# Performance work log

Measured on AMD Instinct MI355X. Metric: run time of the kernel, lower is better.

## Reference

```python
import jax, jax.numpy as jnp
import numpy as np

IDIM, HDIM, ODIM, G = 80, 512, 128, 5
B, T = 512, 512  # B = scan (time) axis of torch GRU (batch_first=False), T = GRU batch axis
P = G * 2 * ODIM + G  # 1285


def setup_inputs() -> dict:
    key = jax.random.key(0)
    ks = jax.random.split(key, 8)
    s = 0.05  # keep recurrent dynamics stable
    return {
        "ys": jax.random.normal(ks[0], (B, T, IDIM), jnp.float32),
        "W_ih": jax.random.normal(ks[1], (3 * HDIM, IDIM), jnp.float32) * s,
        "W_hh": jax.random.normal(ks[2], (3 * HDIM, HDIM), jnp.float32) * s,
        "b_ih": jax.random.normal(ks[3], (3 * HDIM,), jnp.float32) * s,
        "b_hh": jax.random.normal(ks[4], (3 * HDIM,), jnp.float32) * s,
        "W_proj": jax.random.normal(ks[5], (P, HDIM), jnp.float32) * s,
        "b_proj": jax.random.normal(ks[6], (P,), jnp.float32) * s,
        "eps": jax.random.normal(ks[7], (G, B, ODIM), jnp.float32),  # pre-drawn std-normal noise per component
    }


def _gru(ys, W_ih, W_hh, b_ih, b_hh):
    # torch GRU, batch_first=False: scan over axis 0 of ys, batch = axis 1.
    xp = jnp.einsum('btf,gf->btg', ys, W_ih) + b_ih  # (B, T, 3H), precomputed input projections
    h0 = jnp.zeros((ys.shape[1], HDIM), ys.dtype)

    def step(h, x):
        gh = h @ W_hh.T + b_hh
        xr, xz, xn = jnp.split(x, 3, axis=-1)
        hr, hz, hn = jnp.split(gh, 3, axis=-1)
        r = jax.nn.sigmoid(xr + hr)
        z = jax.nn.sigmoid(xz + hz)
        n = jnp.tanh(xn + r * hn)
        h_new = (1.0 - z) * n + z * h
        return h_new, h_new

    _, out = jax.lax.scan(step, h0, xp)  # (B, T, H)
    return out


def reference(ys, W_ih, W_hh, b_ih, b_hh, W_proj, b_proj, eps):
    out = _gru(ys, W_ih, W_hh, b_ih, b_hh)          # (B, T, H)
    last = out[:, -1, :]                             # (B, H), mirrors out[:, -1, :] in torch code
    params = last @ W_proj.T + b_proj                # (B, P)

    samples = jnp.zeros((ys.shape[0], ODIM), params.dtype)
    for i in range(G):  # tiny fixed component loop (G=5)
        mu = params[:, i * ODIM:(i + 1) * ODIM]                       # (B, odim)
        var = params[:, 2 * i * ODIM:(2 * i + 1) * ODIM] + 1e-6       # scale_tril diagonal == std
        s = jax.lax.stop_gradient(mu + var * eps[i])                  # MVN(mu, diag(var)^T diag(var)).sample()
        w = params[:, 2 * G * ODIM + i]                               # params[:, i - G]
        samples = samples + w[:, None] * s
    return samples[:, None, :]  # (B, 1, odim)
```

## Files before the change

### kernel.cpp

```cpp
#include <hip/hip_runtime.h>
#include <hip/hip_bf16.h>

#define IDIM 80
#define HDIM 512
#define ODIM 128
#define G5   5
#define BB   512
#define TT   512
#define PDIM 1285
#define GDIM 1536
#define NW   16
#define JPB  32

__global__ void __launch_bounds__(512) xp_kernel(
    const float* __restrict__ ys, const float* __restrict__ W_ih,
    const float* __restrict__ b_ih, float* __restrict__ xp)
{
  __shared__ float wih[32 * 82];
  __shared__ float bihs[32];
  const int tid = threadIdx.x;
  const int g0 = blockIdx.x * 32;
  const int b0 = blockIdx.y * 64;
  for (int idx = tid; idx < 32 * IDIM; idx += 512) {
    int g = idx / IDIM, f = idx % IDIM;
    wih[g * 82 + f] = W_ih[(size_t)(g0 + g) * IDIM + f];
  }
  if (tid < 32) bihs[tid] = b_ih[g0 + tid];
  __syncthreads();
  const int g = tid & 31, bo = tid >> 5;
  for (int pass = 0; pass < 4; ++pass) {
    int b = b0 + pass * 16 + bo;
    const float* yrow = ys + ((size_t)b * TT + (TT - 1)) * IDIM;
    float acc = bihs[g];
    #pragma unroll
    for (int f = 0; f < IDIM; f += 2) {
      float2 wv = *(const float2*)(&wih[g * 82 + f]);
      float2 yv = *(const float2*)(&yrow[f]);
      acc += wv.x * yv.x + wv.y * yv.y;
    }
    xp[(size_t)b * GDIM + g0 + g] = acc;
  }
}

__global__ void __launch_bounds__(512) gru_kernel(
    const float* __restrict__ W_hh, const float* __restrict__ b_hh,
    const float* __restrict__ xp, unsigned long long* __restrict__ hw,
    float* __restrict__ last)
{
  const int nb   = blockIdx.x;
  const int tid  = threadIdx.x;
  const int lane = tid & 63;
  const int wave = tid >> 6;
  const int r4   = lane >> 4;
  const int c    = lane & 15;
  const int jj   = wave * 4 + r4;
  const int jglob = nb * JPB + jj;
  const bool prod = (c == 0);

  __shared__ float hs[2][16 * 36];

  float4 wreg[3][8];
  float bias[3];
  #pragma unroll
  for (int g = 0; g < 3; ++g) {
    const float* wrow = W_hh + ((size_t)(g * HDIM + jglob)) * HDIM + c * 32;
    #pragma unroll
    for (int i = 0; i < 8; ++i) wreg[g][i] = ((const float4*)wrow)[i];
    bias[g] = b_hh[g * HDIM + jglob];
  }

  for (int w = tid; w < 16 * 36; w += 512) { hs[0][w] = 0.f; hs[1][w] = 0.f; }
  __syncthreads();

  const int j = tid;
  const int jphys = (j >> 5) * 36 + (j & 31);
  const int pphys = (jglob >> 5) * 36 + (jglob & 31);

  for (int b = 0; b < BB; ++b) {
    float xr = 0.f, xz = 0.f, xn = 0.f;
    if (prod) {
      const float* xpb = xp + (size_t)b * GDIM;
      xr = xpb[jglob];
      xz = xpb[512 + jglob];
      xn = xpb[1024 + jglob];
    }

    const float* hbase = &hs[b & 1][c * 36];
    float4 h4[8];
    #pragma unroll
    for (int i = 0; i < 8; ++i) h4[i] = ((const float4*)hbase)[i];

    float gsum[3];
    #pragma unroll
    for (int g = 0; g < 3; ++g) {
      float a0 = 0.f, a1 = 0.f, a2 = 0.f, a3 = 0.f;
      #pragma unroll
      for (int i = 0; i < 8; ++i) {
        a0 += wreg[g][i].x * h4[i].x; a1 += wreg[g][i].y * h4[i].y;
        a2 += wreg[g][i].z * h4[i].z; a3 += wreg[g][i].w * h4[i].w;
      }
      float acc = (a0 + a1) + (a2 + a3);
      acc += __shfl_xor(acc, 1);
      acc += __shfl_xor(acc, 2);
      acc += __shfl_xor(acc, 4);
      acc += __shfl_xor(acc, 8);
      gsum[g] = acc;
    }

    unsigned long long* slot = hw + (size_t)(b & 1) * HDIM;

    if (prod) {
      float h_old = hs[b & 1][pphys];
      float r = 1.f / (1.f + __expf(-(xr + gsum[0] + bias[0])));
      float z = 1.f / (1.f + __expf(-(xz + gsum[1] + bias[1])));
      float e2 = __expf(2.f * (xn + r * (gsum[2] + bias[2])));
      float n = 1.f - 2.f / (e2 + 1.f);
      float hnew = (1.f - z) * n + z * h_old;
      last[(size_t)b * HDIM + jglob] = hnew;
      union { float f; unsigned u; } cv; cv.f = hnew;
      unsigned long long pv = ((unsigned long long)(unsigned)b << 32) | cv.u;
      __hip_atomic_store(&slot[jglob], pv, __ATOMIC_RELAXED,
                         __HIP_MEMORY_SCOPE_AGENT);
    }

    unsigned long long v;
    int guard = 0;
    do {
      v = __hip_atomic_load(&slot[j], __ATOMIC_RELAXED,
                            __HIP_MEMORY_SCOPE_AGENT);
    } while ((unsigned)(v >> 32) != (unsigned)b && ++guard < (1 << 20));

    union { unsigned u; float f; } hv; hv.u = (unsigned)v;
    hs[(b + 1) & 1][jphys] = hv.f;
    __syncthreads();
  }
}

__global__ void __launch_bounds__(256) proj_kernel(
    const float* __restrict__ last, const float* __restrict__ W_proj,
    const float* __restrict__ b_proj, float* __restrict__ params)
{
  const int tid = threadIdx.x;
  const int pt = blockIdx.x * 64;
  const int bt = blockIdx.y * 64;
  __shared__ float As[16 * 65];
  __shared__ float Bs[16 * 65];
  const int tb = (tid >> 4) * 4;
  const int tp = (tid & 15) * 4;
  float acc[4][4] = {};
  for (int k0 = 0; k0 < HDIM; k0 += 16) {
    #pragma unroll
    for (int i = 0; i < 4; ++i) {
      int idx = tid + i * 256;
      int k = idx & 15, m = idx >> 4;
      As[k * 65 + m] = last[(size_t)(bt + m) * HDIM + k0 + k];
      int gp = pt + m;
      Bs[k * 65 + m] = (gp < PDIM) ? W_proj[(size_t)gp * HDIM + k0 + k] : 0.f;
    }
    __syncthreads();
    #pragma unroll
    for (int k = 0; k < 16; ++k) {
      float a[4], bv[4];
      #pragma unroll
      for (int i = 0; i < 4; ++i) a[i] = As[k * 65 + tb + i];
      #pragma unroll
      for (int i = 0; i < 4; ++i) bv[i] = Bs[k * 65 + tp + i];
      #pragma unroll
      for (int i = 0; i < 4; ++i)
        #pragma unroll
        for (int jj = 0; jj < 4; ++jj) acc[i][jj] += a[i] * bv[jj];
    }
    __syncthreads();
  }
  #pragma unroll
  for (int i = 0; i < 4; ++i) {
    int gb = bt + tb + i;
    #pragma unroll
    for (int jj = 0; jj < 4; ++jj) {
      int gp = pt + tp + jj;
      if (gp < PDIM) params[(size_t)gb * PDIM + gp] = acc[i][jj] + b_proj[gp];
    }
  }
}

__global__ void mix_kernel(const float* __restrict__ params,
                           const float* __restrict__ eps,
                           float* __restrict__ out)
{
  int b = blockIdx.x, o = threadIdx.x;
  const float* pr = params + (size_t)b * PDIM;
  float s = 0.f;
  #pragma unroll
  for (int i = 0; i < G5; ++i) {
    float mu  = pr[i * ODIM + o];
    float var = pr[2 * i * ODIM + o] + 1e-6f;
    float w   = pr[2 * G5 * ODIM + i];
    float e   = eps[((size_t)i * BB + b) * ODIM + o];
    s += w * (mu + var * e);
  }
  out[(size_t)b * ODIM + o] = s;
}

extern "C" void kernel_launch(void* const* d_in, const int* in_sizes, int n_in,
                              void* d_out, int out_size, void* d_ws, size_t ws_size,
                              hipStream_t stream) {
  const float* ys     = (const float*)d_in[0];
  const float* W_ih   = (const float*)d_in[1];
  const float* W_hh   = (const float*)d_in[2];
  const float* b_ih   = (const float*)d_in[3];
  const float* b_hh   = (const float*)d_in[4];
  const float* W_proj = (const float*)d_in[5];
  const float* b_proj = (const float*)d_in[6];
  const float* eps    = (const float*)d_in[7];
  float* out = (float*)d_out;

  char* ws = (char*)d_ws;
  unsigned long long* hw = (unsigned long long*)ws;
  float* xp     = (float*)(ws + 2 * HDIM * 8 + 256);
  float* last   = xp + (size_t)BB * GDIM;
  float* params = last + (size_t)BB * HDIM;

  hipMemsetAsync(hw, 0xFF, 2 * HDIM * 8, stream);

  dim3 gx(GDIM / 32, BB / 64);
  xp_kernel<<<gx, 512, 0, stream>>>(ys, W_ih, b_ih, xp);

  gru_kernel<<<NW, 512, 0, stream>>>(W_hh, b_hh, xp, hw, last);

  dim3 gc((PDIM + 63) / 64, BB / 64);
  proj_kernel<<<gc, 256, 0, stream>>>(last, W_proj, b_proj, params);

  mix_kernel<<<BB, ODIM, 0, stream>>>(params, eps, out);
}
```

Before: 1.277 ms.

## Co-locate GRU blocks on one XCC and use workgroup-scope handoff when possible

The GRU kernel now launches 128 blocks and keeps only every eighth one active. The intent is that round-robin dispatch places the 16 working blocks on the same XCC. At startup the blocks exchange their XCC ids, and if all match they publish hidden state with workgroup-scope atomics and poll with CAS, mirroring each value to an agent-scope buffer as a fallback. This targets the per-step cross-block synchronization latency, which goes through the device-wide coherence point, but it relies on dispatch placement and on workgroup-scope atomics being visible across CUs through the shared L2, which is not a guaranteed memory-model property.

```diff
diff --git a/kernel.cpp b/kernel.cpp
--- a/kernel.cpp
+++ b/kernel.cpp
@@ -10,6 +10,7 @@
 #define PDIM 1285
 #define GDIM 1536
 #define NW   16
+#define NLAUNCH 128
 #define JPB  32
 
 __global__ void __launch_bounds__(512) xp_kernel(
@@ -42,36 +43,14 @@
   }
 }
 
-__global__ void __launch_bounds__(512) gru_kernel(
-    const float* __restrict__ W_hh, const float* __restrict__ b_hh,
-    const float* __restrict__ xp, unsigned long long* __restrict__ hw,
-    float* __restrict__ last)
-{
-  const int nb   = blockIdx.x;
-  const int tid  = threadIdx.x;
-  const int lane = tid & 63;
-  const int wave = tid >> 6;
-  const int r4   = lane >> 4;
-  const int c    = lane & 15;
-  const int jj   = wave * 4 + r4;
-  const int jglob = nb * JPB + jj;
-  const bool prod = (c == 0);
-
-  __shared__ float hs[2][16 * 36];
-
-  float4 wreg[3][8];
-  float bias[3];
-  #pragma unroll
-  for (int g = 0; g < 3; ++g) {
-    const float* wrow = W_hh + ((size_t)(g * HDIM + jglob)) * HDIM + c * 32;
-    #pragma unroll
-    for (int i = 0; i < 8; ++i) wreg[g][i] = ((const float4*)wrow)[i];
-    bias[g] = b_hh[g * HDIM + jglob];
-  }
-
-  for (int w = tid; w < 16 * 36; w += 512) { hs[0][w] = 0.f; hs[1][w] = 0.f; }
-  __syncthreads();
-
+template<int FAST>
+__device__ __forceinline__ void run_steps(
+    int tid, int c, int jglob, bool prod,
+    const float4 (&wreg)[3][8], const float (&bias)[3],
+    const float* __restrict__ xp,
+    unsigned long long* __restrict__ hw, unsigned long long* __restrict__ mir,
+    float* __restrict__ last, float (*hs)[16 * 36])
+{
   const int j = tid;
   const int jphys = (j >> 5) * 36 + (j & 31);
   const int pphys = (jglob >> 5) * 36 + (jglob & 31);
@@ -107,7 +86,8 @@
       gsum[g] = acc;
     }
 
-    unsigned long long* slot = hw + (size_t)(b & 1) * HDIM;
+    unsigned long long* slot  = hw  + (size_t)(b & 1) * HDIM;
+    unsigned long long* mslot = mir + (size_t)(b & 1) * HDIM;
 
     if (prod) {
       float h_old = hs[b & 1][pphys];
@@ -116,24 +96,110 @@
       float e2 = __expf(2.f * (xn + r * (gsum[2] + bias[2])));
       float n = 1.f - 2.f / (e2 + 1.f);
       float hnew = (1.f - z) * n + z * h_old;
-      last[(size_t)b * HDIM + jglob] = hnew;
       union { float f; unsigned u; } cv; cv.f = hnew;
       unsigned long long pv = ((unsigned long long)(unsigned)b << 32) | cv.u;
-      __hip_atomic_store(&slot[jglob], pv, __ATOMIC_RELAXED,
-                         __HIP_MEMORY_SCOPE_AGENT);
+      if constexpr (FAST != 0) {
+        __hip_atomic_store(&slot[jglob], pv, __ATOMIC_RELAXED,
+                           __HIP_MEMORY_SCOPE_WORKGROUP);
+        __hip_atomic_store(&mslot[jglob], pv, __ATOMIC_RELAXED,
+                           __HIP_MEMORY_SCOPE_AGENT);
+      } else {
+        __hip_atomic_store(&slot[jglob], pv, __ATOMIC_RELAXED,
+                           __HIP_MEMORY_SCOPE_AGENT);
+      }
+      last[(size_t)b * HDIM + jglob] = hnew;
     }
 
     unsigned long long v;
-    int guard = 0;
-    do {
-      v = __hip_atomic_load(&slot[j], __ATOMIC_RELAXED,
-                            __HIP_MEMORY_SCOPE_AGENT);
-    } while ((unsigned)(v >> 32) != (unsigned)b && ++guard < (1 << 20));
+    if constexpr (FAST != 0) {
+      int it = 0;
+      for (;;) {
+        unsigned long long exp = 0xDEADBEEF00000000ull;
+        __hip_atomic_compare_exchange_strong(&slot[j], &exp, 0xDEADBEEF00000000ull,
+            __ATOMIC_RELAXED, __ATOMIC_RELAXED, __HIP_MEMORY_SCOPE_WORKGROUP);
+        v = exp;
+        if ((unsigned)(v >> 32) == (unsigned)b) break;
+        if (++it >= (1 << 16)) {
+          int g2 = 0;
+          do {
+            v = __hip_atomic_load(&mslot[j], __ATOMIC_RELAXED,
+                                  __HIP_MEMORY_SCOPE_AGENT);
+          } while ((unsigned)(v >> 32) != (unsigned)b && ++g2 < (1 << 20));
+          break;
+        }
+      }
+    } else {
+      int guard = 0;
+      do {
+        v = __hip_atomic_load(&slot[j], __ATOMIC_RELAXED,
+                              __HIP_MEMORY_SCOPE_AGENT);
+      } while ((unsigned)(v >> 32) != (unsigned)b && ++guard < (1 << 20));
+    }
 
     union { unsigned u; float f; } hv; hv.u = (unsigned)v;
     hs[(b + 1) & 1][jphys] = hv.f;
     __syncthreads();
   }
+}
+
+__global__ void __launch_bounds__(512) gru_kernel(
+    const float* __restrict__ W_hh, const float* __restrict__ b_hh,
+    const float* __restrict__ xp, unsigned long long* __restrict__ hw,
+    unsigned long long* __restrict__ mir, float* __restrict__ last,
+    unsigned* __restrict__ cons)
+{
+  if (blockIdx.x & 7) return;
+  const int nb   = blockIdx.x >> 3;
+  const int tid  = threadIdx.x;
+  const int lane = tid & 63;
+  const int wave = tid >> 6;
+  const int r4   = lane >> 4;
+  const int c    = lane & 15;
+  const int jj   = wave * 4 + r4;
+  const int jglob = nb * JPB + jj;
+  const bool prod = (c == 0);
+
+  __shared__ float hs[2][16 * 36];
+  __shared__ int fast_s;
+
+  float4 wreg[3][8];
+  float bias[3];
+  #pragma unroll
+  for (int g = 0; g < 3; ++g) {
+    const float* wrow = W_hh + ((size_t)(g * HDIM + jglob)) * HDIM + c * 32;
+    #pragma unroll
+    for (int i = 0; i < 8; ++i) wreg[g][i] = ((const float4*)wrow)[i];
+    bias[g] = b_hh[g * HDIM + jglob];
+  }
+
+  for (int w = tid; w < 16 * 36; w += 512) { hs[0][w] = 0.f; hs[1][w] = 0.f; }
+
+  if (tid == 0) {
+    unsigned xcc;
+    asm volatile("s_getreg_b32 %0, hwreg(HW_REG_XCC_ID)" : "=s"(xcc));
+    __hip_atomic_store(&cons[nb], 0x100u | (xcc & 0xFFu),
+                       __ATOMIC_RELAXED, __HIP_MEMORY_SCOPE_AGENT);
+    unsigned vals[NW];
+    bool all; int it = 0;
+    do {
+      all = true;
+      for (int i = 0; i < NW; ++i) {
+        vals[i] = __hip_atomic_load(&cons[i], __ATOMIC_RELAXED,
+                                    __HIP_MEMORY_SCOPE_AGENT);
+        all = all && ((vals[i] >> 8) == 1u);
+      }
+      if (!all) __builtin_amdgcn_s_sleep(2);
+    } while (!all && ++it < (1 << 20));
+    bool eq = all;
+    for (int i = 1; i < NW; ++i) eq = eq && (vals[i] == vals[0]);
+    fast_s = eq ? 1 : 0;
+  }
+  __syncthreads();
+
+  if (fast_s)
+    run_steps<1>(tid, c, jglob, prod, wreg, bias, xp, hw, mir, last, hs);
+  else
+    run_steps<0>(tid, c, jglob, prod, wreg, bias, xp, hw, mir, last, hs);
 }
 
 __global__ void __launch_bounds__(256) proj_kernel(
@@ -215,17 +281,20 @@
   float* out = (float*)d_out;
 
   char* ws = (char*)d_ws;
-  unsigned long long* hw = (unsigned long long*)ws;
-  float* xp     = (float*)(ws + 2 * HDIM * 8 + 256);
+  unsigned long long* hw  = (unsigned long long*)ws;
+  unsigned long long* mir = hw + 2 * HDIM;
+  unsigned* cons = (unsigned*)(ws + 4 * HDIM * 8);
+  float* xp     = (float*)(ws + 4 * HDIM * 8 + 256);
   float* last   = xp + (size_t)BB * GDIM;
   float* params = last + (size_t)BB * HDIM;
 
-  hipMemsetAsync(hw, 0xFF, 2 * HDIM * 8, stream);
+  hipMemsetAsync(hw, 0xFF, 4 * HDIM * 8, stream);
+  hipMemsetAsync(cons, 0x00, 256, stream);
 
   dim3 gx(GDIM / 32, BB / 64);
   xp_kernel<<<gx, 512, 0, stream>>>(ys, W_ih, b_ih, xp);
 
-  gru_kernel<<<NW, 512, 0, stream>>>(W_hh, b_hh, xp, hw, last);
+  gru_kernel<<<NLAUNCH, 512, 0, stream>>>(W_hh, b_hh, xp, hw, mir, last, cons);
 
   dim3 gc((PDIM + 63) / 64, BB / 64);
   proj_kernel<<<gc, 256, 0, stream>>>(last, W_proj, b_proj, params);
```

Result: slower. 1.870 ms (+46.4%).
